# Performance work log

Hardware: AMD Instinct MI355X
Metric: run time of the kernel (lower is better)

## Reference

```python
import jax, jax.numpy as jnp
import numpy as np

B, N, D, DS, LAT, FD, NF = 2, 384, 128, 3, 256, 1, 2
NPOS = DS * (2 * 5 + 1)  # 3 + 3*2*5 = 33
FREQS = np.linspace(1.0, 32.0, 5)  # torch.linspace(1, 2**5, 5)
EPS = 1e-5


def _bn(x, g, b):
    # BatchNorm1d, train-mode batch stats: normalize per channel over (batch, points)
    m = jnp.mean(x, axis=(0, 1))
    v = jnp.var(x, axis=(0, 1))
    return (x - m) * jax.lax.rsqrt(v + EPS) * g + b


def _tblock(xyz4, f, Wq, Wk, Wv, Wg1, bg1, Wg2, bg2, Wpe, bpe, g, b):
    # group_all=True full vector attention. f: [B,n,D], xyz4: [B,n,3]
    q = f @ Wq.T
    k = f @ Wk.T
    v = f @ Wv.T
    # knn_xyz gathered under no_grad in torch -> stop_gradient on the key side
    pd = xyz4[:, :, None] - jax.lax.stop_gradient(xyz4)[:, None]  # [B,n,n,3]
    parts = [pd]
    for fr in FREQS:
        parts.append(jnp.sin(pd * fr))
        parts.append(jnp.cos(pd * fr))
    pos = jnp.concatenate(parts, axis=-1) @ Wpe.T + bpe  # [B,n,n,D]
    edges = q[:, :, None] - k[:, None] + pos  # [B,n,n,D]
    h = jax.nn.relu(edges @ Wg1.T + bg1)
    attn = jax.nn.softmax(h @ Wg2.T + bg2, axis=-2)  # softmax over neighbor axis
    res = jnp.sum(attn * (v[:, None] + pos), axis=2)  # einsum bmnf,bmnf->bmf
    return _bn(res + f, g, b)


def setup_inputs() -> dict:
    key = jax.random.key(0)
    ks = iter(jax.random.split(key, 40))
    def rn(shape, s=0.05):
        return jax.random.normal(next(ks), shape, dtype=jnp.float32) * s
    z = lambda *s: jnp.zeros(s, jnp.float32)
    o = lambda *s: jnp.ones(s, jnp.float32)
    nb = NF + 1  # begin block + nfinal blocks
    return {
        "xyz": jax.random.normal(next(ks), (B, N, DS), dtype=jnp.float32),
        "feats": jax.random.normal(next(ks), (B, N, FD), dtype=jnp.float32),
        "enc_W": rn((D, FD)), "enc_b": z(D),
        "tb_Wq": rn((nb, D, D)), "tb_Wk": rn((nb, D, D)), "tb_Wv": rn((nb, D, D)),
        "tb_Wg1": rn((nb, D, D)), "tb_bg1": z(nb, D),
        "tb_Wg2": rn((nb, D, D)), "tb_bg2": z(nb, D),
        "tb_Wpe": rn((nb, D, NPOS)), "tb_bpe": z(nb, D),
        "tb_gamma": o(nb, D), "tb_beta": z(nb, D),
        "em_W1": rn((NF, D, D)), "em_b1": z(NF, D),
        "em_W2": rn((NF, D, D)), "em_b2": z(NF, D),
        "em_gamma": o(NF, D), "em_beta": z(NF, D),
        "fcf_W1": rn((LAT, D)), "fcf_b1": z(LAT),
        "fcf_W2": rn((LAT, LAT)), "fcf_b2": z(LAT),
    }


def reference(xyz, feats, enc_W, enc_b, tb_Wq, tb_Wk, tb_Wv, tb_Wg1, tb_bg1,
              tb_Wg2, tb_bg2, tb_Wpe, tb_bpe, tb_gamma, tb_beta,
              em_W1, em_b1, em_W2, em_b2, em_gamma, em_beta,
              fcf_W1, fcf_b1, fcf_W2, fcf_b2):
    f = feats @ enc_W.T + enc_b  # enc_feats
    x4 = xyz * 4.0
    for i in range(NF + 1):  # i=0: transformer_begin; i>=1: final transformers
        f = _tblock(x4, f, tb_Wq[i], tb_Wk[i], tb_Wv[i], tb_Wg1[i], tb_bg1[i],
                    tb_Wg2[i], tb_bg2[i], tb_Wpe[i], tb_bpe[i], tb_gamma[i], tb_beta[i])
        if i > 0:
            j = i - 1  # ElementwiseMLP: bn(x + relu(conv2(relu(conv1(x)))))
            y = jax.nn.relu(f @ em_W1[j].T + em_b1[j])
            y = jax.nn.relu(y @ em_W2[j].T + em_b2[j])
            f = _bn(f + y, em_gamma[j], em_beta[j])
    e = jax.nn.relu(f @ fcf_W1.T + fcf_b1) @ fcf_W2.T + fcf_b2
    return jnp.max(e, axis=1)  # lat_rep [B, lat_dim]
```

## Files before the change

kernel.cpp:

```cpp
#include <hip/hip_runtime.h>
#include <hip/hip_bf16.h>

#define B_ 2
#define N_ 384
#define D_ 128
#define LAT_ 256
#define NPOS_ 33
#define ROWS_ (B_*N_)
#define NT_ 64
#define ITERS_ (N_/NT_)

typedef __attribute__((ext_vector_type(8))) short bf16x8;
typedef __attribute__((ext_vector_type(4))) float f32x4;

#define MFMA(a,b,c) __builtin_amdgcn_mfma_f32_16x16x32_bf16((a),(b),(c),0,0,0)

__device__ __forceinline__ unsigned short f2bf(float x) {
    unsigned int u = __float_as_uint(x);
    u += 0x7FFFu + ((u >> 16) & 1u);
    return (unsigned short)(u >> 16);
}
__device__ __forceinline__ float bf2f(unsigned short u) {
    return __uint_as_float(((unsigned int)u) << 16);
}

__device__ __forceinline__ float bn_apply(float x, const float* stats, const float* gam,
                                          const float* bet, int d) {
    float s  = stats[d], sq = stats[128 + d];
    float mean = s * (1.f/ROWS_);
    float var  = sq * (1.f/ROWS_) - mean*mean;
    return (x - mean) * rsqrtf(var + 1e-5f) * gam[d] + bet[d];
}

__global__ __launch_bounds__(256) void fprep_kernel(const float* __restrict__ xyz,
                                                    unsigned short* __restrict__ gF) {
    int i = blockIdx.x*256 + threadIdx.x;
    if (i >= ROWS_*64) return;
    int n = i >> 6, q = i & 63;
    float val;
    if (q == 0) val = 1.f;
    else if (q < 4) val = 4.f*xyz[n*3 + (q-1)];
    else if (q < 34) {
        int u = q-4, fi = u/6, rem = u - fi*6, j = rem >> 1;
        const float fr = fi==0?1.f:(fi==1?8.75f:(fi==2?16.5f:(fi==3?24.25f:32.f)));
        float a = fr*4.f*xyz[n*3+j];
        val = (rem & 1) ? __sinf(a) : __cosf(a);
    } else val = 0.f;
    gF[n*64 + (q ^ ((n & 7) << 3))] = f2bf(val);
}

__global__ __launch_bounds__(256) void enc_kernel(const float* __restrict__ feats,
                           const float* __restrict__ W,
                           const float* __restrict__ bias,
                           float* __restrict__ f) {
    int i = blockIdx.x*256 + threadIdx.x;
    if (i >= ROWS_*D_) return;
    int r = i >> 7, d = i & 127;
    f[i] = feats[r]*W[d] + bias[d];
}

__global__ __launch_bounds__(128) void qkv_kernel(const float* __restrict__ graw,
    const float* __restrict__ stats, const float* __restrict__ gam, const float* __restrict__ bet,
    int use_stats,
    const float* __restrict__ Wq, const float* __restrict__ Wk, const float* __restrict__ Wv,
    float* __restrict__ q, unsigned short* __restrict__ k16, unsigned short* __restrict__ v16) {
    __shared__ float rows[4][D_];
    const int r0 = blockIdx.x*4, d = threadIdx.x;
    #pragma unroll
    for (int rr = 0; rr < 4; ++rr) {
        float x = graw[(r0+rr)*D_ + d];
        if (use_stats) x = bn_apply(x, stats, gam, bet, d);
        rows[rr][d] = x;
    }
    __syncthreads();
    float aq[4] = {0,0,0,0}, ak[4] = {0,0,0,0}, av[4] = {0,0,0,0};
    #pragma unroll 4
    for (int e4 = 0; e4 < D_/4; ++e4) {
        float4 wq = *(const float4*)(Wq + d*D_ + e4*4);
        float4 wk = *(const float4*)(Wk + d*D_ + e4*4);
        float4 wv = *(const float4*)(Wv + d*D_ + e4*4);
        #pragma unroll
        for (int rr = 0; rr < 4; ++rr) {
            float4 x = *(const float4*)&rows[rr][e4*4];
            aq[rr] += wq.x*x.x + wq.y*x.y + wq.z*x.z + wq.w*x.w;
            ak[rr] += wk.x*x.x + wk.y*x.y + wk.z*x.z + wk.w*x.w;
            av[rr] += wv.x*x.x + wv.y*x.y + wv.z*x.z + wv.w*x.w;
        }
    }
    #pragma unroll
    for (int rr = 0; rr < 4; ++rr) {
        q[(r0+rr)*D_ + d]   = aq[rr];
        k16[(r0+rr)*D_ + d] = f2bf(ak[rr]);
        v16[(r0+rr)*D_ + d] = f2bf(av[rr]);
    }
}

__global__ __launch_bounds__(512) void attn_mfma_kernel(
    const float* __restrict__ xyz, const float* __restrict__ graw,
    const float* __restrict__ stats_in, const float* __restrict__ gam_in,
    const float* __restrict__ bet_in, int use_stats,
    const float* __restrict__ qb,
    const unsigned short* __restrict__ kb, const unsigned short* __restrict__ vb,
    const unsigned short* __restrict__ gF,
    const float* __restrict__ Wpe, const float* __restrict__ bpe,
    const float* __restrict__ Wg1, const float* __restrict__ bg1,
    const float* __restrict__ Wg2, const float* __restrict__ bg2,
    float* __restrict__ gout, float* __restrict__ stats_out)
{
    __shared__ unsigned short sF[NT_*64];
    __shared__ unsigned short sX[NT_*128];
    __shared__ unsigned short sH[NT_*128];
    __shared__ float sRed[4*128];

    const int t   = threadIdx.x;
    const int w   = t >> 6;
    const int l   = t & 63;
    const int lr  = l & 15;
    const int lg  = l >> 4;
    const int rb2 = w >> 2;
    const int ct0 = (w & 3) * 2;

    const int row  = blockIdx.x;
    const int b    = row / N_;
    const int brow = b * N_;

    uint4 fst = *(const uint4*)(gF + (size_t)brow*64 + t*8);

    float kreg[2][2][4], vreg[2][2][4];
    auto loadK = [&](int n0) {
        #pragma unroll
        for (int rt = 0; rt < 2; ++rt)
        #pragma unroll
        for (int ct = 0; ct < 2; ++ct) {
            const int d = (ct0 + ct)*16 + lr;
            #pragma unroll
            for (int r = 0; r < 4; ++r) {
                const int rr = rb2*32 + rt*16 + lg*4 + r;
                kreg[rt][ct][r] = bf2f(kb[(brow + n0 + rr)*D_ + d]);
            }
        }
    };
    auto loadV = [&](int n0) {
        #pragma unroll
        for (int rt = 0; rt < 2; ++rt)
        #pragma unroll
        for (int ct = 0; ct < 2; ++ct) {
            const int d = (ct0 + ct)*16 + lr;
            #pragma unroll
            for (int r = 0; r < 4; ++r) {
                const int rr = rb2*32 + rt*16 + lg*4 + r;
                vreg[rt][ct][r] = bf2f(vb[(brow + n0 + rr)*D_ + d]);
            }
        }
    };
    loadK(0);

    bf16x8 bWg1[2][4], bWg2[2][4], bG[2][2];
    float  bg1_c[2], bg2_c[2], q_c[2];

    const float xm0 = 4.f*xyz[row*3+0];
    const float xm1 = 4.f*xyz[row*3+1];
    const float xm2 = 4.f*xyz[row*3+2];

    #pragma unroll
    for (int ct = 0; ct < 2; ++ct) {
        const int dout = (ct0 + ct) * 16 + lr;
        #pragma unroll
        for (int kt = 0; kt < 4; ++kt) {
            const float* p1 = Wg1 + dout * D_ + kt * 32 + lg * 8;
            const float* p2 = Wg2 + dout * D_ + kt * 32 + lg * 8;
            float4 a0 = *(const float4*)(p1);
            float4 a1 = *(const float4*)(p1 + 4);
            float4 c0 = *(const float4*)(p2);
            float4 c1 = *(const float4*)(p2 + 4);
            bf16x8 v1, v2;
            v1[0]=(short)f2bf(a0.x); v1[1]=(short)f2bf(a0.y); v1[2]=(short)f2bf(a0.z); v1[3]=(short)f2bf(a0.w);
            v1[4]=(short)f2bf(a1.x); v1[5]=(short)f2bf(a1.y); v1[6]=(short)f2bf(a1.z); v1[7]=(short)f2bf(a1.w);
            v2[0]=(short)f2bf(c0.x); v2[1]=(short)f2bf(c0.y); v2[2]=(short)f2bf(c0.z); v2[3]=(short)f2bf(c0.w);
            v2[4]=(short)f2bf(c1.x); v2[5]=(short)f2bf(c1.y); v2[6]=(short)f2bf(c1.z); v2[7]=(short)f2bf(c1.w);
            bWg1[ct][kt] = v1;
            bWg2[ct][kt] = v2;
        }
        const float* wrow = Wpe + dout*NPOS_;
        float bias = bpe[dout] + wrow[0]*xm0 + wrow[1]*xm1 + wrow[2]*xm2;
        #pragma unroll
        for (int kt = 0; kt < 2; ++kt) {
            bf16x8 g;
            #pragma unroll
            for (int e = 0; e < 8; ++e) {
                const int qq = kt*32 + lg*8 + e;
                float val;
                if (qq == 0) val = bias;
                else if (qq < 4) val = -wrow[qq-1];
                else if (qq < 34) {
                    const int u = qq - 4, fi = u/6, rem = u - fi*6, j = rem >> 1;
                    const float Ws = wrow[3 + 6*fi + j];
                    const float Wc = wrow[3 + 6*fi + 3 + j];
                    const float fr = fi==0?1.f:(fi==1?8.75f:(fi==2?16.5f:(fi==3?24.25f:32.f)));
                    const float am = fr * (j==0?xm0:(j==1?xm1:xm2));
                    const float sm = __sinf(am), cm = __cosf(am);
                    val = (rem & 1) ? (Wc*sm - Ws*cm) : (Ws*sm + Wc*cm);
                } else val = 0.f;
                g[e] = (short)f2bf(val);
            }
            bG[ct][kt] = g;
        }
        bg1_c[ct] = bg1[dout];
        bg2_c[ct] = bg2[dout];
        q_c[ct]   = qb[row*D_ + dout];
    }

    f32x4 pos[2][2];
    auto posedges = [&]() {
        #pragma unroll
        for (int rt = 0; rt < 2; ++rt)
        #pragma unroll
        for (int ct = 0; ct < 2; ++ct) {
            f32x4 acc = {0.f, 0.f, 0.f, 0.f};
            #pragma unroll
            for (int kt = 0; kt < 2; ++kt) {
                const int r16 = rb2*32 + rt*16 + lr;
                const int idx = (r16*64 + kt*32 + lg*8) ^ ((r16 & 7) << 3);
                bf16x8 a = *(const bf16x8*)&sF[idx];
                acc = MFMA(a, bG[ct][kt], acc);
            }
            pos[rt][ct] = acc;
        }
        #pragma unroll
        for (int rt = 0; rt < 2; ++rt)
        #pragma unroll
        for (int ct = 0; ct < 2; ++ct) {
            const int d = (ct0 + ct)*16 + lr;
            #pragma unroll
            for (int r = 0; r < 4; ++r) {
                const int rr = rb2*32 + rt*16 + lg*4 + r;
                const float e = pos[rt][ct][r] + q_c[ct] - kreg[rt][ct][r];
                sX[(rr*128 + d) ^ ((rr & 7) << 3)] = f2bf(e);
            }
        }
    };

    *(uint4*)&sF[t*8] = fst;
    __syncthreads();
    posedges();
    __syncthreads();

    float res_p[2] = {0.f, 0.f}, s_p[2] = {0.f, 0.f};

    for (int it = 0; it < ITERS_; ++it) {
        const int n0 = it * NT_;
        const bool more = (it < ITERS_ - 1);

        if (more) {
            fst = *(const uint4*)(gF + (size_t)(brow + n0 + NT_)*64 + t*8);
            loadK(n0 + NT_);
        }
        loadV(n0);
        f32x4 hacc[2][2];
        #pragma unroll
        for (int rt = 0; rt < 2; ++rt) {
            hacc[rt][0] = (f32x4){bg1_c[0], bg1_c[0], bg1_c[0], bg1_c[0]};
            hacc[rt][1] = (f32x4){bg1_c[1], bg1_c[1], bg1_c[1], bg1_c[1]};
            #pragma unroll
            for (int kt = 0; kt < 4; ++kt) {
                const int r16 = rb2*32 + rt*16 + lr;
                const int idx = (r16*128 + kt*32 + lg*8) ^ ((r16 & 7) << 3);
                bf16x8 a = *(const bf16x8*)&sX[idx];
                hacc[rt][0] = MFMA(a, bWg1[0][kt], hacc[rt][0]);
                hacc[rt][1] = MFMA(a, bWg1[1][kt], hacc[rt][1]);
            }
        }
        #pragma unroll
        for (int rt = 0; rt < 2; ++rt)
        #pragma unroll
        for (int ct = 0; ct < 2; ++ct) {
            const int d = (ct0 + ct)*16 + lr;
            #pragma unroll
            for (int r = 0; r < 4; ++r) {
                const int rr = rb2*32 + rt*16 + lg*4 + r;
                sH[(rr*128 + d) ^ ((rr & 7) << 3)] = f2bf(fmaxf(hacc[rt][ct][r], 0.f));
            }
        }
        if (more) *(uint4*)&sF[t*8] = fst;
        __syncthreads();

        f32x4 lacc[2][2];
        #pragma unroll
        for (int rt = 0; rt < 2; ++rt) {
            lacc[rt][0] = (f32x4){bg2_c[0], bg2_c[0], bg2_c[0], bg2_c[0]};
            lacc[rt][1] = (f32x4){bg2_c[1], bg2_c[1], bg2_c[1], bg2_c[1]};
            #pragma unroll
            for (int kt = 0; kt < 4; ++kt) {
                const int r16 = rb2*32 + rt*16 + lr;
                const int idx = (r16*128 + kt*32 + lg*8) ^ ((r16 & 7) << 3);
                bf16x8 a = *(const bf16x8*)&sH[idx];
                lacc[rt][0] = MFMA(a, bWg2[0][kt], lacc[rt][0]);
                lacc[rt][1] = MFMA(a, bWg2[1][kt], lacc[rt][1]);
            }
        }
        #pragma unroll
        for (int rt = 0; rt < 2; ++rt)
        #pragma unroll
        for (int ct = 0; ct < 2; ++ct) {
            #pragma unroll
            for (int r = 0; r < 4; ++r) {
                const float wgt = __expf(lacc[rt][ct][r]);
                const float vp  = vreg[rt][ct][r] + pos[rt][ct][r];
                res_p[ct] += wgt * vp;
                s_p[ct]   += wgt;
            }
        }
        if (more) {
            posedges();
            __syncthreads();
        }
    }

    #pragma unroll
    for (int ct = 0; ct < 2; ++ct) {
        #pragma unroll
        for (int off = 16; off < 64; off <<= 1) {
            res_p[ct] += __shfl_xor(res_p[ct], off, 64);
            s_p[ct]   += __shfl_xor(s_p[ct], off, 64);
        }
    }
    if (lg == 0) {
        #pragma unroll
        for (int ct = 0; ct < 2; ++ct) {
            const int d = (ct0 + ct)*16 + lr;
            sRed[(rb2*2+0)*128 + d] = res_p[ct];
            sRed[(rb2*2+1)*128 + d] = s_p[ct];
        }
    }
    __syncthreads();
    if (t < D_) {
        const float rsum = sRed[t]       + sRed[2*128 + t];
        const float ssum = sRed[128 + t] + sRed[3*128 + t];
        float fres = graw[row*D_ + t];
        if (use_stats) fres = bn_apply(fres, stats_in, gam_in, bet_in, t);
        const float val = rsum / ssum + fres;
        gout[row*D_ + t] = val;
        atomicAdd(&stats_out[t], val);
        atomicAdd(&stats_out[128 + t], val*val);
    }
}

__global__ __launch_bounds__(128) void em_kernel(const float* __restrict__ graw,
    const float* __restrict__ stats_in, const float* __restrict__ gam_in, const float* __restrict__ bet_in,
    const float* __restrict__ W1, const float* __restrict__ b1,
    const float* __restrict__ W2, const float* __restrict__ b2,
    float* __restrict__ gout, float* __restrict__ stats_out)
{
    __shared__ float rows[4][D_], y1[4][D_];
    const int r0 = blockIdx.x*4, d = threadIdx.x;
    float fn[4];
    #pragma unroll
    for (int rr = 0; rr < 4; ++rr) {
        fn[rr] = bn_apply(graw[(r0+rr)*D_ + d], stats_in, gam_in, bet_in, d);
        rows[rr][d] = fn[rr];
    }
    __syncthreads();
    float a[4] = {b1[d], b1[d], b1[d], b1[d]};
    #pragma unroll 4
    for (int e4 = 0; e4 < D_/4; ++e4) {
        float4 w = *(const float4*)(W1 + d*D_ + e4*4);
        #pragma unroll
        for (int rr = 0; rr < 4; ++rr) {
            float4 x = *(const float4*)&rows[rr][e4*4];
            a[rr] += w.x*x.x + w.y*x.y + w.z*x.z + w.w*x.w;
        }
    }
    #pragma unroll
    for (int rr = 0; rr < 4; ++rr) y1[rr][d] = fmaxf(a[rr], 0.f);
    __syncthreads();
    float a2[4] = {b2[d], b2[d], b2[d], b2[d]};
    #pragma unroll 4
    for (int e4 = 0; e4 < D_/4; ++e4) {
        float4 w = *(const float4*)(W2 + d*D_ + e4*4);
        #pragma unroll
        for (int rr = 0; rr < 4; ++rr) {
            float4 x = *(const float4*)&y1[rr][e4*4];
            a2[rr] += w.x*x.x + w.y*x.y + w.z*x.z + w.w*x.w;
        }
    }
    #pragma unroll
    for (int rr = 0; rr < 4; ++rr) {
        const float g2 = fn[rr] + fmaxf(a2[rr], 0.f);
        gout[(r0+rr)*D_ + d] = g2;
        atomicAdd(&stats_out[d], g2);
        atomicAdd(&stats_out[128+d], g2*g2);
    }
}

__global__ __launch_bounds__(256) void final_kernel(const float* __restrict__ graw,
    const float* __restrict__ stats_in, const float* __restrict__ gam_in, const float* __restrict__ bet_in,
    const float* __restrict__ W1, const float* __restrict__ b1,
    const float* __restrict__ W2, const float* __restrict__ b2,
    float* __restrict__ e_ws)
{
    __shared__ float rows[4][D_];
    __shared__ float h1[4][LAT_];
    const int r0 = blockIdx.x*4, t = threadIdx.x;
    for (int i = t; i < 4*D_; i += 256) {
        const int rr = i >> 7, d = i & 127;
        rows[rr][d] = bn_apply(graw[(r0+rr)*D_ + d], stats_in, gam_in, bet_in, d);
    }
    __syncthreads();
    float a[4] = {b1[t], b1[t], b1[t], b1[t]};
    #pragma unroll 4
    for (int e4 = 0; e4 < D_/4; ++e4) {
        float4 w = *(const float4*)(W1 + t*D_ + e4*4);
        #pragma unroll
        for (int rr = 0; rr < 4; ++rr) {
            float4 x = *(const float4*)&rows[rr][e4*4];
            a[rr] += w.x*x.x + w.y*x.y + w.z*x.z + w.w*x.w;
        }
    }
    #pragma unroll
    for (int rr = 0; rr < 4; ++rr) h1[rr][t] = fmaxf(a[rr], 0.f);
    __syncthreads();
    float a2[4] = {b2[t], b2[t], b2[t], b2[t]};
    #pragma unroll 4
    for (int e4 = 0; e4 < LAT_/4; ++e4) {
        float4 w = *(const float4*)(W2 + t*LAT_ + e4*4);
        #pragma unroll
        for (int rr = 0; rr < 4; ++rr) {
            float4 x = *(const float4*)&h1[rr][e4*4];
            a2[rr] += w.x*x.x + w.y*x.y + w.z*x.z + w.w*x.w;
        }
    }
    #pragma unroll
    for (int rr = 0; rr < 4; ++rr) e_ws[(r0+rr)*LAT_ + t] = a2[rr];
}

__global__ __launch_bounds__(256) void maxred_kernel(const float* __restrict__ e_ws,
                                                     float* __restrict__ out)
{
    int b = blockIdx.x, l = threadIdx.x;
    float m = -INFINITY;
    #pragma unroll 8
    for (int n=0;n<N_;n++) m = fmaxf(m, e_ws[(b*N_+n)*LAT_+l]);
    out[b*LAT_+l] = m;
}

extern "C" void kernel_launch(void* const* d_in, const int* in_sizes, int n_in,
                              void* d_out, int out_size, void* d_ws, size_t ws_size,
                              hipStream_t stream) {
    (void)in_sizes; (void)n_in; (void)out_size; (void)ws_size;
    const float* xyz    = (const float*)d_in[0];
    const float* feats  = (const float*)d_in[1];
    const float* enc_W  = (const float*)d_in[2];
    const float* enc_b  = (const float*)d_in[3];
    const float* tb_Wq  = (const float*)d_in[4];
    const float* tb_Wk  = (const float*)d_in[5];
    const float* tb_Wv  = (const float*)d_in[6];
    const float* tb_Wg1 = (const float*)d_in[7];
    const float* tb_bg1 = (const float*)d_in[8];
    const float* tb_Wg2 = (const float*)d_in[9];
    const float* tb_bg2 = (const float*)d_in[10];
    const float* tb_Wpe = (const float*)d_in[11];
    const float* tb_bpe = (const float*)d_in[12];
    const float* tb_gamma = (const float*)d_in[13];
    const float* tb_beta  = (const float*)d_in[14];
    const float* em_W1  = (const float*)d_in[15];
    const float* em_b1  = (const float*)d_in[16];
    const float* em_W2  = (const float*)d_in[17];
    const float* em_b2  = (const float*)d_in[18];
    const float* em_gamma = (const float*)d_in[19];
    const float* em_beta  = (const float*)d_in[20];
    const float* fcf_W1 = (const float*)d_in[21];
    const float* fcf_b1 = (const float*)d_in[22];
    const float* fcf_W2 = (const float*)d_in[23];
    const float* fcf_b2 = (const float*)d_in[24];
    float* out = (float*)d_out;

    float* ws   = (float*)d_ws;
    float* buf0 = ws;
    float* buf1 = buf0 + ROWS_*D_;
    float* qbuf = buf1 + ROWS_*D_;
    float* ebuf = qbuf + ROWS_*D_;
    float* stats = ebuf + ROWS_*LAT_;
    float* sA0 = stats;
    float* sA1 = stats + 256;
    float* sE1 = stats + 512;
    float* sA2 = stats + 768;
    float* sE2 = stats + 1024;
    unsigned short* kbuf = (unsigned short*)(stats + 5*256);
    unsigned short* vbuf = kbuf + ROWS_*D_;
    unsigned short* gF   = vbuf + ROWS_*D_;

    hipMemsetAsync(stats, 0, 5*256*sizeof(float), stream);

    fprep_kernel<<<(ROWS_*64+255)/256, 256, 0, stream>>>(xyz, gF);
    enc_kernel<<<(ROWS_*D_+255)/256, 256, 0, stream>>>(feats, enc_W, enc_b, buf0);

    const float* gz = tb_gamma;
    qkv_kernel<<<ROWS_/4, 128, 0, stream>>>(buf0, gz, gz, gz, 0,
                                            tb_Wq, tb_Wk, tb_Wv, qbuf, kbuf, vbuf);
    attn_mfma_kernel<<<ROWS_, 512, 0, stream>>>(xyz, buf0, gz, gz, gz, 0,
        qbuf, kbuf, vbuf, gF,
        tb_Wpe, tb_bpe, tb_Wg1, tb_bg1, tb_Wg2, tb_bg2, buf1, sA0);
    qkv_kernel<<<ROWS_/4, 128, 0, stream>>>(buf1, sA0, tb_gamma, tb_beta, 1,
                                            tb_Wq + 1*D_*D_, tb_Wk + 1*D_*D_, tb_Wv + 1*D_*D_,
                                            qbuf, kbuf, vbuf);
    attn_mfma_kernel<<<ROWS_, 512, 0, stream>>>(xyz, buf1, sA0, tb_gamma, tb_beta, 1,
        qbuf, kbuf, vbuf, gF,
        tb_Wpe + 1*D_*NPOS_, tb_bpe + 1*D_, tb_Wg1 + 1*D_*D_, tb_bg1 + 1*D_,
        tb_Wg2 + 1*D_*D_, tb_bg2 + 1*D_, buf0, sA1);
    em_kernel<<<ROWS_/4, 128, 0, stream>>>(buf0, sA1, tb_gamma + 1*D_, tb_beta + 1*D_,
                                           em_W1, em_b1, em_W2, em_b2, buf1, sE1);
    qkv_kernel<<<ROWS_/4, 128, 0, stream>>>(buf1, sE1, em_gamma, em_beta, 1,
                                            tb_Wq + 2*D_*D_, tb_Wk + 2*D_*D_, tb_Wv + 2*D_*D_,
                                            qbuf, kbuf, vbuf);
    attn_mfma_kernel<<<ROWS_, 512, 0, stream>>>(xyz, buf1, sE1, em_gamma, em_beta, 1,
        qbuf, kbuf, vbuf, gF,
        tb_Wpe + 2*D_*NPOS_, tb_bpe + 2*D_, tb_Wg1 + 2*D_*D_, tb_bg1 + 2*D_,
        tb_Wg2 + 2*D_*D_, tb_bg2 + 2*D_, buf0, sA2);
    em_kernel<<<ROWS_/4, 128, 0, stream>>>(buf0, sA2, tb_gamma + 2*D_, tb_beta + 2*D_,
                                           em_W1 + 1*D_*D_, em_b1 + 1*D_,
                                           em_W2 + 1*D_*D_, em_b2 + 1*D_, buf1, sE2);
    final_kernel<<<ROWS_/4, 256, 0, stream>>>(buf1, sE2, em_gamma + 1*D_, em_beta + 1*D_,
                                              fcf_W1, fcf_b1, fcf_W2, fcf_b2, ebuf);
    maxred_kernel<<<B_, 256, 0, stream>>>(ebuf, out);
}
```

Before: 689.3 us.

## Fold Wg1 into q, k and positional weights to drop per-pair Wg1 GEMM

Uses linearity of the first gating layer: Wg1·(q - k + pos) is split into a per-row Wg1·q + bg1, a per-key Wg1·k, and a positional term computed from a precomputed Wg1·Wpe matrix (psi). The per-pair 128x128 Wg1 MFMA over edges becomes a small K=64 MFMA on the Fourier features, alongside the existing positional one. A new psi kernel and extra Wg1 projections in the qkv kernel are added, and the sX staging buffer goes away. The prefetch schedule also changes. Rounding changes because bf16 is now applied to different intermediates.

```diff
diff --git a/kernel.cpp b/kernel.cpp
--- a/kernel.cpp
+++ b/kernel.cpp
@@ -49,6 +49,25 @@
     gF[n*64 + (q ^ ((n & 7) << 3))] = f2bf(val);
 }
 
+__global__ __launch_bounds__(128) void psi_kernel(
+    const float* __restrict__ Wg1, const float* __restrict__ Wpe,
+    const float* __restrict__ bpe, float* __restrict__ psi)
+{
+    const int blk = blockIdx.x, layer = blk / 34, p = blk - layer*34;
+    const float* wg1 = Wg1 + layer*D_*D_;
+    __shared__ float col[D_];
+    const int e = threadIdx.x;
+    col[e] = (p < NPOS_) ? Wpe[layer*D_*NPOS_ + e*NPOS_ + p] : bpe[layer*D_ + e];
+    __syncthreads();
+    float acc = 0.f;
+    #pragma unroll 4
+    for (int d4 = 0; d4 < 32; ++d4) {
+        float4 w = *(const float4*)(wg1 + e*D_ + d4*4);
+        acc += w.x*col[d4*4] + w.y*col[d4*4+1] + w.z*col[d4*4+2] + w.w*col[d4*4+3];
+    }
+    psi[layer*D_*34 + e*34 + p] = acc;
+}
+
 __global__ __launch_bounds__(256) void enc_kernel(const float* __restrict__ feats,
                            const float* __restrict__ W,
                            const float* __restrict__ bias,
@@ -59,12 +78,14 @@
     f[i] = feats[r]*W[d] + bias[d];
 }
 
-__global__ __launch_bounds__(128) void qkv_kernel(const float* __restrict__ graw,
+__global__ __launch_bounds__(128) void qkvkw_kernel(const float* __restrict__ graw,
     const float* __restrict__ stats, const float* __restrict__ gam, const float* __restrict__ bet,
     int use_stats,
     const float* __restrict__ Wq, const float* __restrict__ Wk, const float* __restrict__ Wv,
-    float* __restrict__ q, unsigned short* __restrict__ k16, unsigned short* __restrict__ v16) {
-    __shared__ float rows[4][D_];
+    const float* __restrict__ Wg1, const float* __restrict__ bg1,
+    float* __restrict__ hb, unsigned short* __restrict__ kw16, unsigned short* __restrict__ v16)
+{
+    __shared__ float rows[4][D_], qrows[4][D_], krows[4][D_];
     const int r0 = blockIdx.x*4, d = threadIdx.x;
     #pragma unroll
     for (int rr = 0; rr < 4; ++rr) {
@@ -89,9 +110,29 @@
     }
     #pragma unroll
     for (int rr = 0; rr < 4; ++rr) {
-        q[(r0+rr)*D_ + d]   = aq[rr];
-        k16[(r0+rr)*D_ + d] = f2bf(ak[rr]);
         v16[(r0+rr)*D_ + d] = f2bf(av[rr]);
+        qrows[rr][d] = aq[rr];
+        krows[rr][d] = ak[rr];
+    }
+    __syncthreads();
+    float hq[4], hk[4] = {0,0,0,0};
+    #pragma unroll
+    for (int rr = 0; rr < 4; ++rr) hq[rr] = bg1[d];
+    #pragma unroll 4
+    for (int e4 = 0; e4 < D_/4; ++e4) {
+        float4 w = *(const float4*)(Wg1 + d*D_ + e4*4);
+        #pragma unroll
+        for (int rr = 0; rr < 4; ++rr) {
+            float4 xq = *(const float4*)&qrows[rr][e4*4];
+            float4 xk = *(const float4*)&krows[rr][e4*4];
+            hq[rr] += w.x*xq.x + w.y*xq.y + w.z*xq.z + w.w*xq.w;
+            hk[rr] += w.x*xk.x + w.y*xk.y + w.z*xk.z + w.w*xk.w;
+        }
+    }
+    #pragma unroll
+    for (int rr = 0; rr < 4; ++rr) {
+        hb[(r0+rr)*D_ + d]   = hq[rr];
+        kw16[(r0+rr)*D_ + d] = f2bf(hk[rr]);
     }
 }
 
@@ -99,16 +140,15 @@
     const float* __restrict__ xyz, const float* __restrict__ graw,
     const float* __restrict__ stats_in, const float* __restrict__ gam_in,
     const float* __restrict__ bet_in, int use_stats,
-    const float* __restrict__ qb,
-    const unsigned short* __restrict__ kb, const unsigned short* __restrict__ vb,
+    const float* __restrict__ hbb,
+    const unsigned short* __restrict__ kwb, const unsigned short* __restrict__ vb,
     const unsigned short* __restrict__ gF,
+    const float* __restrict__ psiL,
     const float* __restrict__ Wpe, const float* __restrict__ bpe,
-    const float* __restrict__ Wg1, const float* __restrict__ bg1,
     const float* __restrict__ Wg2, const float* __restrict__ bg2,
     float* __restrict__ gout, float* __restrict__ stats_out)
 {
     __shared__ unsigned short sF[NT_*64];
-    __shared__ unsigned short sX[NT_*128];
     __shared__ unsigned short sH[NT_*128];
     __shared__ float sRed[4*128];
 
@@ -124,10 +164,10 @@
     const int b    = row / N_;
     const int brow = b * N_;
 
-    uint4 fst = *(const uint4*)(gF + (size_t)brow*64 + t*8);
-
-    float kreg[2][2][4], vreg[2][2][4];
-    auto loadK = [&](int n0) {
+    uint4 freg = *(const uint4*)(gF + (size_t)brow*64 + t*8);
+    unsigned short kw_us[2][2][4];
+    unsigned short v_us[2][2][4];
+    auto loadKW = [&](int n0) {
         #pragma unroll
         for (int rt = 0; rt < 2; ++rt)
         #pragma unroll
@@ -136,7 +176,7 @@
             #pragma unroll
             for (int r = 0; r < 4; ++r) {
                 const int rr = rb2*32 + rt*16 + lg*4 + r;
-                kreg[rt][ct][r] = bf2f(kb[(brow + n0 + rr)*D_ + d]);
+                kw_us[rt][ct][r] = kwb[(brow + n0 + rr)*D_ + d];
             }
         }
     };
@@ -149,14 +189,14 @@
             #pragma unroll
             for (int r = 0; r < 4; ++r) {
                 const int rr = rb2*32 + rt*16 + lg*4 + r;
-                vreg[rt][ct][r] = bf2f(vb[(brow + n0 + rr)*D_ + d]);
+                v_us[rt][ct][r] = vb[(brow + n0 + rr)*D_ + d];
             }
         }
     };
-    loadK(0);
-
-    bf16x8 bWg1[2][4], bWg2[2][4], bG[2][2];
-    float  bg1_c[2], bg2_c[2], q_c[2];
+    loadKW(0);
+
+    bf16x8 bWg2[2][4], bG[2][2], bT[2][2];
+    float  hb_c[2], bg2_c[2];
 
     const float xm0 = 4.f*xyz[row*3+0];
     const float xm1 = 4.f*xyz[row*3+1];
@@ -167,107 +207,94 @@
         const int dout = (ct0 + ct) * 16 + lr;
         #pragma unroll
         for (int kt = 0; kt < 4; ++kt) {
-            const float* p1 = Wg1 + dout * D_ + kt * 32 + lg * 8;
             const float* p2 = Wg2 + dout * D_ + kt * 32 + lg * 8;
-            float4 a0 = *(const float4*)(p1);
-            float4 a1 = *(const float4*)(p1 + 4);
             float4 c0 = *(const float4*)(p2);
             float4 c1 = *(const float4*)(p2 + 4);
-            bf16x8 v1, v2;
-            v1[0]=(short)f2bf(a0.x); v1[1]=(short)f2bf(a0.y); v1[2]=(short)f2bf(a0.z); v1[3]=(short)f2bf(a0.w);
-            v1[4]=(short)f2bf(a1.x); v1[5]=(short)f2bf(a1.y); v1[6]=(short)f2bf(a1.z); v1[7]=(short)f2bf(a1.w);
+            bf16x8 v2;
             v2[0]=(short)f2bf(c0.x); v2[1]=(short)f2bf(c0.y); v2[2]=(short)f2bf(c0.z); v2[3]=(short)f2bf(c0.w);
             v2[4]=(short)f2bf(c1.x); v2[5]=(short)f2bf(c1.y); v2[6]=(short)f2bf(c1.z); v2[7]=(short)f2bf(c1.w);
-            bWg1[ct][kt] = v1;
             bWg2[ct][kt] = v2;
         }
-        const float* wrow = Wpe + dout*NPOS_;
-        float bias = bpe[dout] + wrow[0]*xm0 + wrow[1]*xm1 + wrow[2]*xm2;
-        #pragma unroll
-        for (int kt = 0; kt < 2; ++kt) {
-            bf16x8 g;
-            #pragma unroll
-            for (int e = 0; e < 8; ++e) {
-                const int qq = kt*32 + lg*8 + e;
-                float val;
-                if (qq == 0) val = bias;
-                else if (qq < 4) val = -wrow[qq-1];
-                else if (qq < 34) {
-                    const int u = qq - 4, fi = u/6, rem = u - fi*6, j = rem >> 1;
-                    const float Ws = wrow[3 + 6*fi + j];
-                    const float Wc = wrow[3 + 6*fi + 3 + j];
-                    const float fr = fi==0?1.f:(fi==1?8.75f:(fi==2?16.5f:(fi==3?24.25f:32.f)));
-                    const float am = fr * (j==0?xm0:(j==1?xm1:xm2));
-                    const float sm = __sinf(am), cm = __cosf(am);
-                    val = (rem & 1) ? (Wc*sm - Ws*cm) : (Ws*sm + Wc*cm);
-                } else val = 0.f;
-                g[e] = (short)f2bf(val);
-            }
-            bG[ct][kt] = g;
-        }
-        bg1_c[ct] = bg1[dout];
+        {
+            const float* wrow = Wpe + dout*NPOS_;
+            float bias = bpe[dout] + wrow[0]*xm0 + wrow[1]*xm1 + wrow[2]*xm2;
+            #pragma unroll
+            for (int kt = 0; kt < 2; ++kt) {
+                bf16x8 g;
+                #pragma unroll
+                for (int e = 0; e < 8; ++e) {
+                    const int qq = kt*32 + lg*8 + e;
+                    float val;
+                    if (qq == 0) val = bias;
+                    else if (qq < 4) val = -wrow[qq-1];
+                    else if (qq < 34) {
+                        const int u = qq - 4, fi = u/6, rem = u - fi*6, j = rem >> 1;
+                        const float Ws = wrow[3 + 6*fi + j];
+                        const float Wc = wrow[3 + 6*fi + 3 + j];
+                        const float fr = fi==0?1.f:(fi==1?8.75f:(fi==2?16.5f:(fi==3?24.25f:32.f)));
+                        const float am = fr * (j==0?xm0:(j==1?xm1:xm2));
+                        const float sm = __sinf(am), cm = __cosf(am);
+                        val = (rem & 1) ? (Wc*sm - Ws*cm) : (Ws*sm + Wc*cm);
+                    } else val = 0.f;
+                    g[e] = (short)f2bf(val);
+                }
+                bG[ct][kt] = g;
+            }
+        }
+        {
+            const float* prow = psiL + dout*34;
+            float bias = prow[33] + prow[0]*xm0 + prow[1]*xm1 + prow[2]*xm2;
+            #pragma unroll
+            for (int kt = 0; kt < 2; ++kt) {
+                bf16x8 g;
+                #pragma unroll
+                for (int e = 0; e < 8; ++e) {
+                    const int qq = kt*32 + lg*8 + e;
+                    float val;
+                    if (qq == 0) val = bias;
+                    else if (qq < 4) val = -prow[qq-1];
+                    else if (qq < 34) {
+                        const int u = qq - 4, fi = u/6, rem = u - fi*6, j = rem >> 1;
+                        const float Ws = prow[3 + 6*fi + j];
+                        const float Wc = prow[3 + 6*fi + 3 + j];
+                        const float fr = fi==0?1.f:(fi==1?8.75f:(fi==2?16.5f:(fi==3?24.25f:32.f)));
+                        const float am = fr * (j==0?xm0:(j==1?xm1:xm2));
+                        const float sm = __sinf(am), cm = __cosf(am);
+                        val = (rem & 1) ? (Wc*sm - Ws*cm) : (Ws*sm + Wc*cm);
+                    } else val = 0.f;
+                    g[e] = (short)f2bf(val);
+                }
+                bT[ct][kt] = g;
+            }
+        }
+        hb_c[ct]  = hbb[row*D_ + dout];
         bg2_c[ct] = bg2[dout];
-        q_c[ct]   = qb[row*D_ + dout];
-    }
-
+    }
+
+    *(uint4*)&sF[t*8] = freg;
+    __syncthreads();
+
+    float res_p[2] = {0.f, 0.f}, s_p[2] = {0.f, 0.f};
     f32x4 pos[2][2];
-    auto posedges = [&]() {
-        #pragma unroll
-        for (int rt = 0; rt < 2; ++rt)
-        #pragma unroll
-        for (int ct = 0; ct < 2; ++ct) {
-            f32x4 acc = {0.f, 0.f, 0.f, 0.f};
-            #pragma unroll
-            for (int kt = 0; kt < 2; ++kt) {
-                const int r16 = rb2*32 + rt*16 + lr;
-                const int idx = (r16*64 + kt*32 + lg*8) ^ ((r16 & 7) << 3);
-                bf16x8 a = *(const bf16x8*)&sF[idx];
-                acc = MFMA(a, bG[ct][kt], acc);
-            }
-            pos[rt][ct] = acc;
-        }
-        #pragma unroll
-        for (int rt = 0; rt < 2; ++rt)
-        #pragma unroll
-        for (int ct = 0; ct < 2; ++ct) {
-            const int d = (ct0 + ct)*16 + lr;
-            #pragma unroll
-            for (int r = 0; r < 4; ++r) {
-                const int rr = rb2*32 + rt*16 + lg*4 + r;
-                const float e = pos[rt][ct][r] + q_c[ct] - kreg[rt][ct][r];
-                sX[(rr*128 + d) ^ ((rr & 7) << 3)] = f2bf(e);
-            }
-        }
-    };
-
-    *(uint4*)&sF[t*8] = fst;
-    __syncthreads();
-    posedges();
-    __syncthreads();
-
-    float res_p[2] = {0.f, 0.f}, s_p[2] = {0.f, 0.f};
 
     for (int it = 0; it < ITERS_; ++it) {
         const int n0 = it * NT_;
         const bool more = (it < ITERS_ - 1);
 
-        if (more) {
-            fst = *(const uint4*)(gF + (size_t)(brow + n0 + NT_)*64 + t*8);
-            loadK(n0 + NT_);
-        }
         loadV(n0);
+        if (more) freg = *(const uint4*)(gF + (size_t)(brow + n0 + NT_)*64 + t*8);
         f32x4 hacc[2][2];
         #pragma unroll
         for (int rt = 0; rt < 2; ++rt) {
-            hacc[rt][0] = (f32x4){bg1_c[0], bg1_c[0], bg1_c[0], bg1_c[0]};
-            hacc[rt][1] = (f32x4){bg1_c[1], bg1_c[1], bg1_c[1], bg1_c[1]};
-            #pragma unroll
-            for (int kt = 0; kt < 4; ++kt) {
-                const int r16 = rb2*32 + rt*16 + lr;
-                const int idx = (r16*128 + kt*32 + lg*8) ^ ((r16 & 7) << 3);
-                bf16x8 a = *(const bf16x8*)&sX[idx];
-                hacc[rt][0] = MFMA(a, bWg1[0][kt], hacc[rt][0]);
-                hacc[rt][1] = MFMA(a, bWg1[1][kt], hacc[rt][1]);
+            const int r16 = rb2*32 + rt*16 + lr;
+            const int sw  = (r16 & 7) << 3;
+            bf16x8 a0 = *(const bf16x8*)&sF[(r16*64 +  0 + lg*8) ^ sw];
+            bf16x8 a1 = *(const bf16x8*)&sF[(r16*64 + 32 + lg*8) ^ sw];
+            #pragma unroll
+            for (int ct = 0; ct < 2; ++ct) {
+                f32x4 z = {0.f,0.f,0.f,0.f};
+                hacc[rt][ct] = MFMA(a1, bT[ct][1], MFMA(a0, bT[ct][0], z));
+                pos[rt][ct]  = MFMA(a1, bG[ct][1], MFMA(a0, bG[ct][0], z));
             }
         }
         #pragma unroll
@@ -278,12 +305,16 @@
             #pragma unroll
             for (int r = 0; r < 4; ++r) {
                 const int rr = rb2*32 + rt*16 + lg*4 + r;
-                sH[(rr*128 + d) ^ ((rr & 7) << 3)] = f2bf(fmaxf(hacc[rt][ct][r], 0.f));
-            }
-        }
-        if (more) *(uint4*)&sF[t*8] = fst;
+                const float hv = hacc[rt][ct][r] + hb_c[ct] - bf2f(kw_us[rt][ct][r]);
+                sH[(rr*128 + d) ^ ((rr & 7) << 3)] = f2bf(fmaxf(hv, 0.f));
+            }
+        }
         __syncthreads();
 
+        if (more) {
+            *(uint4*)&sF[t*8] = freg;
+            loadKW(n0 + NT_);
+        }
         f32x4 lacc[2][2];
         #pragma unroll
         for (int rt = 0; rt < 2; ++rt) {
@@ -305,15 +336,12 @@
             #pragma unroll
             for (int r = 0; r < 4; ++r) {
                 const float wgt = __expf(lacc[rt][ct][r]);
-                const float vp  = vreg[rt][ct][r] + pos[rt][ct][r];
+                const float vp  = bf2f(v_us[rt][ct][r]) + pos[rt][ct][r];
                 res_p[ct] += wgt * vp;
                 s_p[ct]   += wgt;
             }
         }
-        if (more) {
-            posedges();
-            __syncthreads();
-        }
+        __syncthreads();
     }
 
     #pragma unroll
@@ -477,45 +505,45 @@
     float* ws   = (float*)d_ws;
     float* buf0 = ws;
     float* buf1 = buf0 + ROWS_*D_;
-    float* qbuf = buf1 + ROWS_*D_;
-    float* ebuf = qbuf + ROWS_*D_;
-    float* stats = ebuf + ROWS_*LAT_;
+    float* hbb  = buf1 + ROWS_*D_;
+    float* ebuf = hbb  + ROWS_*D_;
+    float* psi  = ebuf + ROWS_*LAT_;
+    float* stats = psi + 3*D_*34;
     float* sA0 = stats;
     float* sA1 = stats + 256;
     float* sE1 = stats + 512;
     float* sA2 = stats + 768;
     float* sE2 = stats + 1024;
-    unsigned short* kbuf = (unsigned short*)(stats + 5*256);
-    unsigned short* vbuf = kbuf + ROWS_*D_;
-    unsigned short* gF   = vbuf + ROWS_*D_;
+    unsigned short* kwbuf = (unsigned short*)(stats + 5*256);
+    unsigned short* vbuf  = kwbuf + ROWS_*D_;
+    unsigned short* gF    = vbuf + ROWS_*D_;
 
     hipMemsetAsync(stats, 0, 5*256*sizeof(float), stream);
 
     fprep_kernel<<<(ROWS_*64+255)/256, 256, 0, stream>>>(xyz, gF);
+    psi_kernel<<<3*34, 128, 0, stream>>>(tb_Wg1, tb_Wpe, tb_bpe, psi);
     enc_kernel<<<(ROWS_*D_+255)/256, 256, 0, stream>>>(feats, enc_W, enc_b, buf0);
 
     const float* gz = tb_gamma;
-    qkv_kernel<<<ROWS_/4, 128, 0, stream>>>(buf0, gz, gz, gz, 0,
-                                            tb_Wq, tb_Wk, tb_Wv, qbuf, kbuf, vbuf);
+    qkvkw_kernel<<<ROWS_/4, 128, 0, stream>>>(buf0, gz, gz, gz, 0,
+        tb_Wq, tb_Wk, tb_Wv, tb_Wg1, tb_bg1, hbb, kwbuf, vbuf);
     attn_mfma_kernel<<<ROWS_, 512, 0, stream>>>(xyz, buf0, gz, gz, gz, 0,
-        qbuf, kbuf, vbuf, gF,
-        tb_Wpe, tb_bpe, tb_Wg1, tb_bg1, tb_Wg2, tb_bg2, buf1, sA0);
-    qkv_kernel<<<ROWS_/4, 128, 0, stream>>>(buf1, sA0, tb_gamma, tb_beta, 1,
-                                            tb_Wq + 1*D_*D_, tb_Wk + 1*D_*D_, tb_Wv + 1*D_*D_,
-                                            qbuf, kbuf, vbuf);
+        hbb, kwbuf, vbuf, gF, psi,
+        tb_Wpe, tb_bpe, tb_Wg2, tb_bg2, buf1, sA0);
+    qkvkw_kernel<<<ROWS_/4, 128, 0, stream>>>(buf1, sA0, tb_gamma, tb_beta, 1,
+        tb_Wq + 1*D_*D_, tb_Wk + 1*D_*D_, tb_Wv + 1*D_*D_,
+        tb_Wg1 + 1*D_*D_, tb_bg1 + 1*D_, hbb, kwbuf, vbuf);
     attn_mfma_kernel<<<ROWS_, 512, 0, stream>>>(xyz, buf1, sA0, tb_gamma, tb_beta, 1,
-        qbuf, kbuf, vbuf, gF,
-        tb_Wpe + 1*D_*NPOS_, tb_bpe + 1*D_, tb_Wg1 + 1*D_*D_, tb_bg1 + 1*D_,
-        tb_Wg2 + 1*D_*D_, tb_bg2 + 1*D_, buf0, sA1);
+        hbb, kwbuf, vbuf, gF, psi + 1*D_*34,
+        tb_Wpe + 1*D_*NPOS_, tb_bpe + 1*D_, tb_Wg2 + 1*D_*D_, tb_bg2 + 1*D_, buf0, sA1);
     em_kernel<<<ROWS_/4, 128, 0, stream>>>(buf0, sA1, tb_gamma + 1*D_, tb_beta + 1*D_,
                                            em_W1, em_b1, em_W2, em_b2, buf1, sE1);
-    qkv_kernel<<<ROWS_/4, 128, 0, stream>>>(buf1, sE1, em_gamma, em_beta, 1,
-                                            tb_Wq + 2*D_*D_, tb_Wk + 2*D_*D_, tb_Wv + 2*D_*D_,
-                                            qbuf, kbuf, vbuf);
+    qkvkw_kernel<<<ROWS_/4, 128, 0, stream>>>(buf1, sE1, em_gamma, em_beta, 1,
+        tb_Wq + 2*D_*D_, tb_Wk + 2*D_*D_, tb_Wv + 2*D_*D_,
+        tb_Wg1 + 2*D_*D_, tb_bg1 + 2*D_, hbb, kwbuf, vbuf);
     attn_mfma_kernel<<<ROWS_, 512, 0, stream>>>(xyz, buf1, sE1, em_gamma, em_beta, 1,
-        qbuf, kbuf, vbuf, gF,
-        tb_Wpe + 2*D_*NPOS_, tb_bpe + 2*D_, tb_Wg1 + 2*D_*D_, tb_bg1 + 2*D_,
-        tb_Wg2 + 2*D_*D_, tb_bg2 + 2*D_, buf0, sA2);
+        hbb, kwbuf, vbuf, gF, psi + 2*D_*34,
+        tb_Wpe + 2*D_*NPOS_, tb_bpe + 2*D_, tb_Wg2 + 2*D_*D_, tb_bg2 + 2*D_, buf0, sA2);
     em_kernel<<<ROWS_/4, 128, 0, stream>>>(buf0, sA2, tb_gamma + 2*D_, tb_beta + 2*D_,
                                            em_W1 + 1*D_*D_, em_b1 + 1*D_,
                                            em_W2 + 1*D_*D_, em_b2 + 1*D_, buf1, sE2);
```

Measured after the change: 556.9 us. 1.24x faster.
